# Performance work log

Hardware: AMD Instinct MI355X
Metric: run time of the kernel (lower is better)

The kernel has to match this reference:

```python
import jax, jax.numpy as jnp
import numpy as np

B, T = 16, 2048
V, E, H, C = 32000, 512, 4, 3  # vocab, embed, heads, context (history 2 + current)
EPS = 1e-5


def setup_inputs() -> dict:
    key = jax.random.key(0)
    k0, k1, k2, k3, k4, k5, k6 = jax.random.split(key, 7)
    tokens = jax.random.randint(k0, (B, T), 0, V)
    embed_table = jax.random.normal(k1, (V, E), dtype=jnp.float32)
    pos = jax.random.normal(k2, (H, E, C), dtype=jnp.float32) * (1.0 / np.sqrt(H))
    ffn_w = jax.random.normal(k3, (E, E), dtype=jnp.float32) * (1.0 / np.sqrt(E))
    ffn_b = jax.random.normal(k4, (E,), dtype=jnp.float32) * 0.01
    ln_g = jnp.ones((E,), dtype=jnp.float32)
    ln_b = jnp.zeros((E,), dtype=jnp.float32)
    return {"tokens": tokens, "embed_table": embed_table, "pos": pos,
            "ffn_w": ffn_w, "ffn_b": ffn_b, "ln_g": ln_g, "ln_b": ln_b}


def reference(tokens, embed_table, pos, ffn_w, ffn_b, ln_g, ln_b):
    # embed lookup: [B, T, E]
    x = embed_table[tokens]
    # prepend zero history, extract sliding windows of size C: [B, T, C, E]
    x_cat = jnp.concatenate([jnp.zeros((B, C - 1, E), dtype=x.dtype), x], axis=1)
    x_win = jnp.stack([x_cat[:, i:i + T] for i in range(C)], axis=2)
    # multi-head positional scores: pos viewed as [H, C, E]
    pos_hce = jnp.transpose(pos, (0, 2, 1))  # [H, C, E]
    w = jnp.einsum('btce,hce->bthc', x_win, pos_hce)          # scores
    out = jnp.einsum('bthc,btce->bte', w, x_win) / (H * C)    # weighted sum
    # FFN (torch Linear: y = x @ W^T + b)
    out = out @ ffn_w.T + ffn_b
    # LayerNorm
    mu = jnp.mean(out, axis=-1, keepdims=True)
    var = jnp.mean(jnp.square(out - mu), axis=-1, keepdims=True)
    out = (out - mu) * jax.lax.rsqrt(var + EPS) * ln_g + ln_b
    # swish
    return out * jax.nn.sigmoid(out)
```

## Files before the change

### kernel.cpp

```cpp
#include <hip/hip_runtime.h>
#include <hip/hip_bf16.h>


#define Bq 16
#define Tq 2048
#define Eq 512
#define Cq 3
#define Hq 4
#define Mq (Bq * Tq)
#define LN_EPS 1e-5f

typedef __attribute__((ext_vector_type(8))) short bf16x8;
typedef __attribute__((ext_vector_type(4))) float f32x4;
typedef __attribute__((ext_vector_type(8))) unsigned short u16x8;

__device__ __forceinline__ unsigned short f2bf(float f) {
    unsigned int u = __float_as_uint(f);
    u += 0x7fffu + ((u >> 16) & 1u);
    return (unsigned short)(u >> 16);
}
__device__ __forceinline__ float bf2f(unsigned short h) {
    return __uint_as_float(((unsigned int)h) << 16);
}

__global__ void prep_kernel(const float* __restrict__ pos,
                            const float* __restrict__ ffn_w,
                            float* __restrict__ Pt,
                            unsigned short* __restrict__ Wb) {
    int i = blockIdx.x * blockDim.x + threadIdx.x;
    if (i < Cq * Eq) {
        int c = i / Eq, e = i % Eq;
        float s = 0.f;
#pragma unroll
        for (int h = 0; h < Hq; ++h) s += pos[(h * Eq + e) * Cq + c];
        Pt[i] = s;
    }
    int nth = blockDim.x * gridDim.x;
    for (int j = i; j < Eq * Eq; j += nth) Wb[j] = f2bf(ffn_w[j]);
}

__global__ __launch_bounds__(512, 4) void fused_kernel(const int* __restrict__ tokens,
                                                       const float* __restrict__ tbl,
                                                       const float* __restrict__ Pt,
                                                       const unsigned short* __restrict__ Wb,
                                                       const float* __restrict__ bias,
                                                       const float* __restrict__ ln_g,
                                                       const float* __restrict__ ln_b,
                                                       float* __restrict__ out) {
    __shared__ __align__(16) unsigned short Atile[64 * 512];
    __shared__ float lds_sum[64][8];
    __shared__ float lds_sq[64][8];
    __shared__ float lds_mu[64];
    __shared__ float lds_rs[64];

    const int tid = threadIdx.x;
    const int wave = tid >> 6;
    const int lane = tid & 63;
    const int lr = lane & 15;
    const int lg = lane >> 4;
    const int m0 = blockIdx.x << 6;
    const int b = m0 >> 11;
    const int t0w = (m0 & (Tq - 1)) + (wave << 3);

    float4 pA[Cq], pB[Cq];
#pragma unroll
    for (int c = 0; c < Cq; ++c) {
        const float4* pp = reinterpret_cast<const float4*>(Pt + c * Eq + lane * 8);
        pA[c] = pp[0]; pB[c] = pp[1];
    }

    u16x8 xb[10];
    float d[10][Cq];
    const int tbase = b << 11;
#pragma unroll
    for (int li = 0; li < 10; ++li) {
        const int t = t0w - 2 + li;
        float4 v0 = {0.f, 0.f, 0.f, 0.f}, v1 = {0.f, 0.f, 0.f, 0.f};
        if (t >= 0) {
            const int tok = tokens[tbase + t];
            const float4* rp = reinterpret_cast<const float4*>(tbl + (long)tok * Eq + lane * 8);
            v0 = rp[0]; v1 = rp[1];
        }
#pragma unroll
        for (int c = 0; c < Cq; ++c) {
            d[li][c] = v0.x * pA[c].x + v0.y * pA[c].y + v0.z * pA[c].z + v0.w * pA[c].w
                     + v1.x * pB[c].x + v1.y * pB[c].y + v1.z * pB[c].z + v1.w * pB[c].w;
        }
        u16x8 xv;
        xv[0] = f2bf(v0.x); xv[1] = f2bf(v0.y); xv[2] = f2bf(v0.z); xv[3] = f2bf(v0.w);
        xv[4] = f2bf(v1.x); xv[5] = f2bf(v1.y); xv[6] = f2bf(v1.z); xv[7] = f2bf(v1.w);
        xb[li] = xv;
    }
#pragma unroll
    for (int li = 0; li < 10; ++li) {
#pragma unroll
        for (int c = 0; c < Cq; ++c) {
            if (li >= c && li - c <= 7) {
#pragma unroll
                for (int m = 1; m < 64; m <<= 1) d[li][c] += __shfl_xor(d[li][c], m, 64);
            }
        }
    }
    const float inv = 1.f / (Hq * Cq);
#pragma unroll
    for (int j = 0; j < 8; ++j) {
        const float s0 = d[j][0] * inv, s1 = d[j + 1][1] * inv, s2 = d[j + 2][2] * inv;
        u16x8 o;
#pragma unroll
        for (int e = 0; e < 8; ++e) {
            const float a = s0 * bf2f((unsigned short)xb[j][e])
                          + s1 * bf2f((unsigned short)xb[j + 1][e])
                          + s2 * bf2f((unsigned short)xb[j + 2][e]);
            o[e] = f2bf(a);
        }
        const int row = (wave << 3) + j;
        const int phys = row * 1024 + ((lane * 16) ^ ((row & 7) << 4));
        *reinterpret_cast<u16x8*>(reinterpret_cast<char*>(Atile) + phys) = o;
    }
    __syncthreads();

    const int n0 = wave << 6;
    const short* Bp = reinterpret_cast<const short*>(Wb) + (long)n0 * Eq;

    f32x4 acc[4][4];
#pragma unroll
    for (int i = 0; i < 4; ++i)
#pragma unroll
        for (int j = 0; j < 4; ++j) acc[i][j] = (f32x4){0.f, 0.f, 0.f, 0.f};

#pragma unroll
    for (int kb = 0; kb < 8; ++kb) {
#pragma unroll
        for (int ks = 0; ks < 2; ++ks) {
            bf16x8 af[4], bfv[4];
#pragma unroll
            for (int mf = 0; mf < 4; ++mf) {
                const int r = mf * 16 + lr;
                const int phys = r * 1024 + ((kb * 128 + ks * 64 + lg * 16) ^ ((r & 7) << 4));
                af[mf] = *reinterpret_cast<const bf16x8*>(reinterpret_cast<const char*>(Atile) + phys);
            }
#pragma unroll
            for (int nf = 0; nf < 4; ++nf)
                bfv[nf] = *reinterpret_cast<const bf16x8*>(Bp + (nf * 16 + lr) * Eq + kb * 64 + ks * 32 + lg * 8);
#pragma unroll
            for (int mf = 0; mf < 4; ++mf)
#pragma unroll
                for (int nf = 0; nf < 4; ++nf)
                    acc[mf][nf] = __builtin_amdgcn_mfma_f32_16x16x32_bf16(af[mf], bfv[nf], acc[mf][nf], 0, 0, 0);
        }
    }

    float bcol[4];
#pragma unroll
    for (int nf = 0; nf < 4; ++nf) bcol[nf] = bias[n0 + nf * 16 + lr];

#pragma unroll
    for (int mf = 0; mf < 4; ++mf) {
#pragma unroll
        for (int i = 0; i < 4; ++i) {
            float sm = 0.f, sq = 0.f;
#pragma unroll
            for (int nf = 0; nf < 4; ++nf) {
                float v = acc[mf][nf][i] + bcol[nf];
                acc[mf][nf][i] = v;
                sm += v;
                sq += v * v;
            }
#pragma unroll
            for (int msk = 1; msk < 16; msk <<= 1) {
                sm += __shfl_xor(sm, msk, 64);
                sq += __shfl_xor(sq, msk, 64);
            }
            if (lr == 0) {
                const int row = mf * 16 + lg * 4 + i;
                lds_sum[row][wave] = sm;
                lds_sq[row][wave] = sq;
            }
        }
    }
    __syncthreads();
    if (tid < 64) {
        float sm = 0.f, sq = 0.f;
#pragma unroll
        for (int w = 0; w < 8; ++w) { sm += lds_sum[tid][w]; sq += lds_sq[tid][w]; }
        const float mu = sm * (1.f / Eq);
        const float var = sq * (1.f / Eq) - mu * mu;
        lds_mu[tid] = mu;
        lds_rs[tid] = rsqrtf(var + LN_EPS);
    }
    __syncthreads();

    float gcol[4], bbcol[4];
#pragma unroll
    for (int nf = 0; nf < 4; ++nf) {
        gcol[nf] = ln_g[n0 + nf * 16 + lr];
        bbcol[nf] = ln_b[n0 + nf * 16 + lr];
    }
#pragma unroll
    for (int mf = 0; mf < 4; ++mf) {
#pragma unroll
        for (int i = 0; i < 4; ++i) {
            const int row = mf * 16 + lg * 4 + i;
            const float mu = lds_mu[row];
            const float rs = lds_rs[row];
#pragma unroll
            for (int nf = 0; nf < 4; ++nf) {
                float v = acc[mf][nf][i];
                float o = (v - mu) * rs * gcol[nf] + bbcol[nf];
                o = o / (1.f + __expf(-o));
                out[(long)(m0 + row) * Eq + (n0 + nf * 16 + lr)] = o;
            }
        }
    }
}

extern "C" void kernel_launch(void* const* d_in, const int* in_sizes, int n_in,
                              void* d_out, int out_size, void* d_ws, size_t ws_size,
                              hipStream_t stream) {
    const int* tokens = (const int*)d_in[0];
    const float* tbl = (const float*)d_in[1];
    const float* pos = (const float*)d_in[2];
    const float* ffn_w = (const float*)d_in[3];
    const float* ffn_b = (const float*)d_in[4];
    const float* ln_g = (const float*)d_in[5];
    const float* ln_b = (const float*)d_in[6];
    float* out = (float*)d_out;

    char* ws = (char*)d_ws;
    float* Pt = (float*)ws;
    unsigned short* Wb = (unsigned short*)(ws + 8192);

    hipLaunchKernelGGL(prep_kernel, dim3(64), dim3(256), 0, stream, pos, ffn_w, Pt, Wb);
    hipLaunchKernelGGL(fused_kernel, dim3(Mq / 64), dim3(512), 0, stream,
                       tokens, tbl, Pt, Wb, ffn_b, ln_g, ln_b, out);
}
```

Measured before the change: 74.80 us.

## Prefetch FFN weight fragments early and double-buffer across k-blocks

Weight fragments for the first two k-blocks are loaded before the embedding and score phase, and the GEMM loop prefetches the fragments two k-blocks ahead into a double-buffered register array. This is meant to hide global-memory latency of the weight loads behind earlier work. The embedding rows are also kept in fp32 registers instead of being rounded to bf16 before the weighted sum, and the sum is packed with the v_cvt_pk_bf16_f32 instruction. Launch bounds drop from 4 to 2 blocks per CU to leave room for the extra registers, which may reduce occupancy.

Result: faster. 72.05 us (-3.7%).

```diff
diff --git a/kernel.cpp b/kernel.cpp
--- a/kernel.cpp
+++ b/kernel.cpp
@@ -12,15 +12,19 @@
 
 typedef __attribute__((ext_vector_type(8))) short bf16x8;
 typedef __attribute__((ext_vector_type(4))) float f32x4;
-typedef __attribute__((ext_vector_type(8))) unsigned short u16x8;
 
 __device__ __forceinline__ unsigned short f2bf(float f) {
     unsigned int u = __float_as_uint(f);
     u += 0x7fffu + ((u >> 16) & 1u);
     return (unsigned short)(u >> 16);
 }
-__device__ __forceinline__ float bf2f(unsigned short h) {
-    return __uint_as_float(((unsigned int)h) << 16);
+__device__ __forceinline__ unsigned int cvt_pk_bf16(float lo, float hi) {
+    unsigned int r;
+    asm("v_cvt_pk_bf16_f32 %0, %1, %2" : "=v"(r) : "v"(lo), "v"(hi));
+    return r;
+}
+__device__ __forceinline__ int xaddr(int row, int kbyte) {
+    return row * 1024 + (kbyte ^ ((row & 7) << 4));
 }
 
 __global__ void prep_kernel(const float* __restrict__ pos,
@@ -39,7 +43,7 @@
     for (int j = i; j < Eq * Eq; j += nth) Wb[j] = f2bf(ffn_w[j]);
 }
 
-__global__ __launch_bounds__(512, 4) void fused_kernel(const int* __restrict__ tokens,
+__global__ __launch_bounds__(512, 2) void fused_kernel(const int* __restrict__ tokens,
                                                        const float* __restrict__ tbl,
                                                        const float* __restrict__ Pt,
                                                        const unsigned short* __restrict__ Wb,
@@ -59,69 +63,82 @@
     const int lr = lane & 15;
     const int lg = lane >> 4;
     const int m0 = blockIdx.x << 6;
-    const int b = m0 >> 11;
     const int t0w = (m0 & (Tq - 1)) + (wave << 3);
-
-    float4 pA[Cq], pB[Cq];
-#pragma unroll
-    for (int c = 0; c < Cq; ++c) {
-        const float4* pp = reinterpret_cast<const float4*>(Pt + c * Eq + lane * 8);
-        pA[c] = pp[0]; pB[c] = pp[1];
-    }
-
-    u16x8 xb[10];
-    float d[10][Cq];
-    const int tbase = b << 11;
+    const int tb = (m0 >> 11) << 11;
+    char* Xc = reinterpret_cast<char*>(Atile);
+
+    const int n0 = wave << 6;
+    const short* Bp = reinterpret_cast<const short*>(Wb) + (long)n0 * Eq;
+
+    float x[10][8];
 #pragma unroll
     for (int li = 0; li < 10; ++li) {
         const int t = t0w - 2 + li;
         float4 v0 = {0.f, 0.f, 0.f, 0.f}, v1 = {0.f, 0.f, 0.f, 0.f};
         if (t >= 0) {
-            const int tok = tokens[tbase + t];
+            const int tok = tokens[tb + t];
             const float4* rp = reinterpret_cast<const float4*>(tbl + (long)tok * Eq + lane * 8);
             v0 = rp[0]; v1 = rp[1];
         }
-#pragma unroll
-        for (int c = 0; c < Cq; ++c) {
-            d[li][c] = v0.x * pA[c].x + v0.y * pA[c].y + v0.z * pA[c].z + v0.w * pA[c].w
-                     + v1.x * pB[c].x + v1.y * pB[c].y + v1.z * pB[c].z + v1.w * pB[c].w;
-        }
-        u16x8 xv;
-        xv[0] = f2bf(v0.x); xv[1] = f2bf(v0.y); xv[2] = f2bf(v0.z); xv[3] = f2bf(v0.w);
-        xv[4] = f2bf(v1.x); xv[5] = f2bf(v1.y); xv[6] = f2bf(v1.z); xv[7] = f2bf(v1.w);
-        xb[li] = xv;
-    }
-#pragma unroll
-    for (int li = 0; li < 10; ++li) {
-#pragma unroll
-        for (int c = 0; c < Cq; ++c) {
+        x[li][0] = v0.x; x[li][1] = v0.y; x[li][2] = v0.z; x[li][3] = v0.w;
+        x[li][4] = v1.x; x[li][5] = v1.y; x[li][6] = v1.z; x[li][7] = v1.w;
+    }
+
+    bf16x8 br[2][8];
+#pragma unroll
+    for (int ks = 0; ks < 2; ++ks)
+#pragma unroll
+        for (int nf = 0; nf < 4; ++nf) {
+            br[0][ks * 4 + nf] = *reinterpret_cast<const bf16x8*>(Bp + (nf * 16 + lr) * Eq + 0 * 64 + ks * 32 + lg * 8);
+            br[1][ks * 4 + nf] = *reinterpret_cast<const bf16x8*>(Bp + (nf * 16 + lr) * Eq + 1 * 64 + ks * 32 + lg * 8);
+        }
+
+    float pv[Cq][8];
+#pragma unroll
+    for (int c = 0; c < Cq; ++c) {
+        const float4* pp = reinterpret_cast<const float4*>(Pt + c * Eq + lane * 8);
+        float4 p0 = pp[0], p1 = pp[1];
+        pv[c][0] = p0.x; pv[c][1] = p0.y; pv[c][2] = p0.z; pv[c][3] = p0.w;
+        pv[c][4] = p1.x; pv[c][5] = p1.y; pv[c][6] = p1.z; pv[c][7] = p1.w;
+    }
+    float d[10][Cq];
+#pragma unroll
+    for (int li = 0; li < 10; ++li)
+#pragma unroll
+        for (int c = 0; c < Cq; ++c)
             if (li >= c && li - c <= 7) {
+                float s = 0.f;
+#pragma unroll
+                for (int e = 0; e < 8; ++e) s += x[li][e] * pv[c][e];
+                d[li][c] = s;
+            }
+#pragma unroll
+    for (int li = 0; li < 10; ++li)
+#pragma unroll
+        for (int c = 0; c < Cq; ++c)
+            if (li >= c && li - c <= 7) {
 #pragma unroll
                 for (int m = 1; m < 64; m <<= 1) d[li][c] += __shfl_xor(d[li][c], m, 64);
             }
-        }
-    }
+
     const float inv = 1.f / (Hq * Cq);
 #pragma unroll
-    for (int j = 0; j < 8; ++j) {
-        const float s0 = d[j][0] * inv, s1 = d[j + 1][1] * inv, s2 = d[j + 2][2] * inv;
-        u16x8 o;
-#pragma unroll
-        for (int e = 0; e < 8; ++e) {
-            const float a = s0 * bf2f((unsigned short)xb[j][e])
-                          + s1 * bf2f((unsigned short)xb[j + 1][e])
-                          + s2 * bf2f((unsigned short)xb[j + 2][e]);
-            o[e] = f2bf(a);
-        }
-        const int row = (wave << 3) + j;
-        const int phys = row * 1024 + ((lane * 16) ^ ((row & 7) << 4));
-        *reinterpret_cast<u16x8*>(reinterpret_cast<char*>(Atile) + phys) = o;
+    for (int jj = 0; jj < 8; ++jj) {
+        const float s0 = d[jj][0] * inv, s1 = d[jj + 1][1] * inv, s2 = d[jj + 2][2] * inv;
+        float a[8];
+#pragma unroll
+        for (int e = 0; e < 8; ++e)
+            a[e] = s0 * x[jj][e] + s1 * x[jj + 1][e] + s2 * x[jj + 2][e];
+        uint4 o;
+        o.x = cvt_pk_bf16(a[0], a[1]);
+        o.y = cvt_pk_bf16(a[2], a[3]);
+        o.z = cvt_pk_bf16(a[4], a[5]);
+        o.w = cvt_pk_bf16(a[6], a[7]);
+        const int row = (wave << 3) + jj;
+        *reinterpret_cast<uint4*>(Xc + xaddr(row, lane * 16)) = o;
     }
     __syncthreads();
 
-    const int n0 = wave << 6;
-    const short* Bp = reinterpret_cast<const short*>(Wb) + (long)n0 * Eq;
-
     f32x4 acc[4][4];
 #pragma unroll
     for (int i = 0; i < 4; ++i)
@@ -132,21 +149,24 @@
     for (int kb = 0; kb < 8; ++kb) {
 #pragma unroll
         for (int ks = 0; ks < 2; ++ks) {
-            bf16x8 af[4], bfv[4];
+            bf16x8 af[4];
 #pragma unroll
             for (int mf = 0; mf < 4; ++mf) {
                 const int r = mf * 16 + lr;
-                const int phys = r * 1024 + ((kb * 128 + ks * 64 + lg * 16) ^ ((r & 7) << 4));
-                af[mf] = *reinterpret_cast<const bf16x8*>(reinterpret_cast<const char*>(Atile) + phys);
-            }
-#pragma unroll
-            for (int nf = 0; nf < 4; ++nf)
-                bfv[nf] = *reinterpret_cast<const bf16x8*>(Bp + (nf * 16 + lr) * Eq + kb * 64 + ks * 32 + lg * 8);
+                af[mf] = *reinterpret_cast<const bf16x8*>(Xc + xaddr(r, kb * 128 + ks * 64 + lg * 16));
+            }
 #pragma unroll
             for (int mf = 0; mf < 4; ++mf)
 #pragma unroll
                 for (int nf = 0; nf < 4; ++nf)
-                    acc[mf][nf] = __builtin_amdgcn_mfma_f32_16x16x32_bf16(af[mf], bfv[nf], acc[mf][nf], 0, 0, 0);
+                    acc[mf][nf] = __builtin_amdgcn_mfma_f32_16x16x32_bf16(af[mf], br[kb & 1][ks * 4 + nf], acc[mf][nf], 0, 0, 0);
+        }
+        if (kb < 6) {
+#pragma unroll
+            for (int ks = 0; ks < 2; ++ks)
+#pragma unroll
+                for (int nf = 0; nf < 4; ++nf)
+                    br[kb & 1][ks * 4 + nf] = *reinterpret_cast<const bf16x8*>(Bp + (nf * 16 + lr) * Eq + (kb + 2) * 64 + ks * 32 + lg * 8);
         }
     }
 
```
